# Performance work log

Measured on AMD Instinct MI355X. Metric: run time of the kernel, lower is better.

The kernel has to match this reference:

```python
import jax, jax.numpy as jnp
from jax import lax
import numpy as np

VOCAB = 36906
WORD_DIM = 300
HIDDEN = 200
B = 256
S = 256

def setup_inputs() -> dict:
    key = jax.random.key(0)
    ks = jax.random.split(key, 9)
    premise = jax.random.randint(ks[0], (B, S), 0, VOCAB)
    hypothesis = jax.random.randint(ks[1], (B, S), 0, VOCAB)
    s = 0.05
    emb = jax.random.normal(ks[2], (VOCAB, WORD_DIM), dtype=jnp.float32) * s
    W_ih = jax.random.normal(ks[3], (4 * HIDDEN, WORD_DIM), dtype=jnp.float32) * s
    W_hh = jax.random.normal(ks[4], (4 * HIDDEN, HIDDEN), dtype=jnp.float32) * s
    b_ih = jax.random.normal(ks[5], (4 * HIDDEN,), dtype=jnp.float32) * s
    b_hh = jax.random.normal(ks[6], (4 * HIDDEN,), dtype=jnp.float32) * s
    W_last = jax.random.normal(ks[7], (3, 4 * HIDDEN), dtype=jnp.float32) * s
    b_last = jax.random.normal(ks[8], (3,), dtype=jnp.float32) * s
    return {"premise": premise, "hypothesis": hypothesis, "emb": emb,
            "W_ih": W_ih, "W_hh": W_hh, "b_ih": b_ih, "b_hh": b_hh,
            "W_last": W_last, "b_last": b_last}

def _lstm_hidden_matrix(x_emb, W_ih, W_hh, b_ih, b_hh):
    # x_emb: [B, S, D] -> hidden states [B, S, H] (PyTorch LSTMCell math, zero init state)
    Bz = x_emb.shape[0]
    H = W_hh.shape[1]
    xs = jnp.swapaxes(x_emb, 0, 1)  # [S, B, D]
    h0 = jnp.zeros((Bz, H), x_emb.dtype)
    def step(carry, x_t):
        h, c = carry
        gates = x_t @ W_ih.T + b_ih + h @ W_hh.T + b_hh  # [B, 4H]
        i, f, g, o = jnp.split(gates, 4, axis=1)
        c = jax.nn.sigmoid(f) * c + jax.nn.sigmoid(i) * jnp.tanh(g)
        h = jax.nn.sigmoid(o) * jnp.tanh(c)
        return (h, c), h
    _, hs = lax.scan(step, (h0, h0), xs)
    return jnp.swapaxes(hs, 0, 1)  # [B, S, H]

def reference(premise, hypothesis, emb, W_ih, W_hh, b_ih, b_hh, W_last, b_last):
    _i = _lstm_hidden_matrix(emb[premise], W_ih, W_hh, b_ih, b_hh)      # [B, S, H]
    _t = _lstm_hidden_matrix(emb[hypothesis], W_ih, W_hh, b_ih, b_hh)  # [B, S, H]
    attn = jnp.einsum('bih,bjh->bij', _i, _t)          # [B, S, S]
    a1 = jax.nn.softmax(attn, axis=2)
    hq = jnp.max(jnp.einsum('bij,bjh->bih', a1, _t), axis=1)  # [B, H]
    a2 = jax.nn.softmax(jnp.swapaxes(attn, 1, 2), axis=2)
    hs = jnp.max(jnp.einsum('bji,bih->bjh', a2, _i), axis=1)  # [B, H]
    feat = jnp.concatenate([hq, hs, hq - hs, hq * hs], axis=1)  # [B, 4H]
    logits = feat @ W_last.T + b_last
    return jax.nn.log_softmax(logits, axis=1)
```

## Files before the change

kernel.cpp:

```cpp
#include <hip/hip_runtime.h>

typedef unsigned short u16;
typedef __attribute__((ext_vector_type(8))) __bf16 bf16x8;
typedef __attribute__((ext_vector_type(4))) float float4v;
typedef __attribute__((ext_vector_type(4))) u16 ushort4v;
typedef __attribute__((ext_vector_type(4))) unsigned int uint4v;

#define VOCAB 36906
#define VPAD  36928
#define WDP   320
#define HID   200
#define NG    800
#define NGP   832
#define KP    224
#define SS    256
#define ROWS  4
#define HS    232
#define GSF   804
#define WLS   228
#define NREG  5
#define NLDS  10

__device__ __forceinline__ float b2f(u16 u) {
  union { unsigned int i; float f; } c; c.i = ((unsigned int)u) << 16; return c.f;
}
__device__ __forceinline__ u16 f2b(float f) {
  union { float f; unsigned int i; } c; c.f = f;
  unsigned int u = c.i;
  u += 0x7fffu + ((u >> 16) & 1u);
  return (u16)(u >> 16);
}
__device__ __forceinline__ float sigm(float x) { return 1.f / (1.f + __expf(-x)); }
__device__ __forceinline__ float tanh_f(float x) {
  float e = __expf(2.f * x);
  return 1.f - 2.f / (e + 1.f);
}


__global__ void conv_emb(const float* __restrict__ emb, u16* __restrict__ out) {
  for (long long idx = (long long)blockIdx.x * 256 + threadIdx.x;
       idx < (long long)VPAD * WDP; idx += (long long)gridDim.x * 256) {
    int v = (int)(idx / WDP), k = (int)(idx % WDP);
    float val = (v < VOCAB && k < 300) ? emb[(long long)v * 300 + k] : 0.f;
    out[idx] = f2b(val);
  }
}

__global__ void conv_wih(const float* __restrict__ W, u16* __restrict__ out) {
  int idx = blockIdx.x * 256 + threadIdx.x;
  if (idx < NGP * WDP) {
    int n = idx / WDP, k = idx % WDP;
    float v = 0.f;
    if (n < NG && k < 300) { int gt = n & 3, j = n >> 2; v = W[(gt * HID + j) * 300 + k]; }
    out[idx] = f2b(v);
  }
}

__global__ void conv_whh(const float* __restrict__ W, u16* __restrict__ out) {
  int idx = blockIdx.x * 256 + threadIdx.x;
  if (idx < NG * KP) {
    int n = idx / KP, k = idx % KP;
    int gt = n & 3, j = n >> 2;
    float v = (k < HID) ? W[(gt * HID + j) * HID + k] : 0.f;
    out[idx] = f2b(v);
  }
}

__global__ void conv_bias(const float* __restrict__ bi, const float* __restrict__ bh,
                          float* __restrict__ out) {
  int n = blockIdx.x * 256 + threadIdx.x;
  if (n < NGP) {
    float v = 0.f;
    if (n < NG) { int gt = n & 3, j = n >> 2; v = bi[gt * HID + j] + bh[gt * HID + j]; }
    out[n] = v;
  }
}


__global__ __launch_bounds__(256, 2) void gemm_e2(
    const u16* __restrict__ A, const u16* __restrict__ B, u16* __restrict__ C,
    const float* __restrict__ bias) {
  __shared__ __align__(16) u16 La[64 * 40];
  __shared__ __align__(16) u16 Lb[64 * 40];
  const int m0 = blockIdx.x * 64, n0 = blockIdx.y * 64;
  const int tid = threadIdx.x, l = tid & 63, w = tid >> 6;
  const int wr = w >> 1, wc = w & 1;
  const int sr = tid >> 2, sc = (tid & 3) * 8;
  float4v acc[2][2] = {};
  for (int k0 = 0; k0 < WDP; k0 += 32) {
    uint4v qa = *(const uint4v*)&A[(long long)(m0 + sr) * WDP + k0 + sc];
    uint4v qb = *(const uint4v*)&B[(long long)(n0 + sr) * WDP + k0 + sc];
    __syncthreads();
    *(uint4v*)&La[sr * 40 + sc] = qa;
    *(uint4v*)&Lb[sr * 40 + sc] = qb;
    __syncthreads();
    bf16x8 af[2], bfr[2];
#pragma unroll
    for (int mt = 0; mt < 2; ++mt)
      af[mt] = *(const bf16x8*)&La[(wr * 32 + mt * 16 + (l & 15)) * 40 + (l >> 4) * 8];
#pragma unroll
    for (int nt = 0; nt < 2; ++nt)
      bfr[nt] = *(const bf16x8*)&Lb[(wc * 32 + nt * 16 + (l & 15)) * 40 + (l >> 4) * 8];
#pragma unroll
    for (int mt = 0; mt < 2; ++mt)
#pragma unroll
      for (int nt = 0; nt < 2; ++nt)
        acc[mt][nt] = __builtin_amdgcn_mfma_f32_16x16x32_bf16(af[mt], bfr[nt], acc[mt][nt], 0, 0, 0);
  }
#pragma unroll
  for (int mt = 0; mt < 2; ++mt)
#pragma unroll
    for (int nt = 0; nt < 2; ++nt)
#pragma unroll
      for (int j = 0; j < 4; ++j) {
        int row = m0 + wr * 32 + mt * 16 + (l >> 4) * 4 + j;
        int col = n0 + wc * 32 + nt * 16 + (l & 15);
        if (row < VOCAB && col < NG)
          C[(long long)row * NG + col] = f2b(acc[mt][nt][j] + bias[col]);
      }
}


__global__ __launch_bounds__(512, 2) void lstm_kernel(
    const int* __restrict__ premise, const int* __restrict__ hypothesis,
    const u16* __restrict__ E2, const u16* __restrict__ Whh,
    u16* __restrict__ hid) {
  __shared__ u16 tok[ROWS * 256];
  __shared__ __align__(16) u16 hbuf[16 * HS];
  __shared__ __align__(16) float gbufF[16 * GSF];
  __shared__ __align__(16) u16 wlds[NLDS * 16 * WLS];
  const int tid = threadIdx.x;
  const int l = tid & 63, w = tid >> 6;
  const int r0 = blockIdx.x * ROWS;

  for (int idx = tid; idx < ROWS * 256; idx += 512) {
    int mm = idx >> 8, tt = idx & 255;
    int row = r0 + mm;
    const int* seq = (row < 256) ? premise : hypothesis;
    tok[idx] = (u16)seq[(row & 255) * 256 + tt];
  }
  for (int idx = tid; idx < 16 * HS; idx += 512) hbuf[idx] = 0;
  for (int idx = tid; idx < NLDS * 16 * KP; idx += 512) {
    int slot = idx / (16 * KP), rem = idx % (16 * KP);
    int r = rem / KP, k = rem % KP;
    wlds[(slot * 16 + r) * WLS + k] = Whh[((40 + slot) * 16 + r) * KP + k];
  }

  uint4v wf[NREG][7];
#pragma unroll
  for (int i = 0; i < NREG; ++i) {
    int nt = w + 8 * i;
#pragma unroll
    for (int kf = 0; kf < 7; ++kf)
      wf[i][kf] = *(const uint4v*)&Whh[(nt * 16 + (l & 15)) * KP + kf * 32 + (l >> 4) * 8];
  }
#pragma unroll
  for (int i = 0; i < NREG; ++i)
#pragma unroll
    for (int kf = 0; kf < 7; ++kf)
      asm volatile("" : "+a"(wf[i][kf]));

  float cst[2];
  cst[0] = cst[1] = 0.f;

  ushort4v ev[2];
#pragma unroll
  for (int q = 0; q < 2; ++q) {
    int u = tid + 512 * q;
    if (u < ROWS * 200) {
      int m = u / 200, j = u - m * 200;
      int tk = tok[m * 256];
      ev[q] = *(const ushort4v*)&E2[(long long)tk * NG + 4 * j];
    }
  }
  __syncthreads();

  for (int t = 0; t < SS; ++t) {
    if (t > 0) {
      const unsigned* hb32 = (const unsigned*)hbuf;
      unsigned* hid32 = (unsigned*)hid;
      if (tid < ROWS * 112) {
        int m2 = tid / 112, c = tid - 112 * m2;
        hid32[((long long)(r0 + m2) * SS + (t - 1)) * 112 + c] = hb32[m2 * 116 + c];
      }
    }

    int t2 = (t < SS - 1) ? t + 1 : t;
    ushort4v evn[2];
#pragma unroll
    for (int q = 0; q < 2; ++q) {
      int u = tid + 512 * q;
      if (u < ROWS * 200) {
        int m = u / 200, j = u - m * 200;
        int tk = tok[m * 256 + t2];
        evn[q] = *(const ushort4v*)&E2[(long long)tk * NG + 4 * j];
      }
    }

    bf16x8 af[7];
#pragma unroll
    for (int kf = 0; kf < 7; ++kf)
      af[kf] = *(const bf16x8*)&hbuf[(l & 15) * HS + kf * 32 + (l >> 4) * 8];

    {
      float4v acc[NREG];
#pragma unroll
      for (int i = 0; i < NREG; ++i) acc[i] = float4v{0.f, 0.f, 0.f, 0.f};
      asm volatile("s_nop 1"
                   : "+v"(acc[0]), "+v"(acc[1]), "+v"(acc[2]), "+v"(acc[3]), "+v"(acc[4]));
#pragma unroll
      for (int kf = 0; kf < 7; ++kf)
#pragma unroll
        for (int i = 0; i < NREG; ++i)
          asm volatile("v_mfma_f32_16x16x32_bf16 %0, %1, %2, %0"
                       : "+v"(acc[i])
                       : "a"(wf[i][kf]), "v"(af[kf]));
      asm volatile("s_nop 7\n\ts_nop 7"
                   : "+v"(acc[0]), "+v"(acc[1]), "+v"(acc[2]), "+v"(acc[3]), "+v"(acc[4]));
#pragma unroll
      for (int i = 0; i < NREG; ++i) {
        int nt = w + 8 * i;
        *(float4v*)&gbufF[(l & 15) * GSF + nt * 16 + (l >> 4) * 4] = acc[i];
      }
    }
    {
      float4v a2 = {0.f, 0.f, 0.f, 0.f};
#pragma unroll
      for (int kf = 0; kf < 7; ++kf) {
        bf16x8 bfr = *(const bf16x8*)&wlds[(w * 16 + (l & 15)) * WLS + kf * 32 + (l >> 4) * 8];
        a2 = __builtin_amdgcn_mfma_f32_16x16x32_bf16(bfr, af[kf], a2, 0, 0, 0);
      }
      *(float4v*)&gbufF[(l & 15) * GSF + (40 + w) * 16 + (l >> 4) * 4] = a2;
    }
    if (w < 2) {
      int slot = 8 + w;
      float4v a2 = {0.f, 0.f, 0.f, 0.f};
#pragma unroll
      for (int kf = 0; kf < 7; ++kf) {
        bf16x8 bfr = *(const bf16x8*)&wlds[(slot * 16 + (l & 15)) * WLS + kf * 32 + (l >> 4) * 8];
        a2 = __builtin_amdgcn_mfma_f32_16x16x32_bf16(bfr, af[kf], a2, 0, 0, 0);
      }
      *(float4v*)&gbufF[(l & 15) * GSF + (48 + w) * 16 + (l >> 4) * 4] = a2;
    }
    __syncthreads();

#pragma unroll
    for (int q = 0; q < 2; ++q) {
      int u = tid + 512 * q;
      if (u < ROWS * 200) {
        int m = u / 200, j = u - m * 200;
        float4v gv = *(const float4v*)&gbufF[m * GSF + 4 * j];
        float gi = gv[0] + b2f(ev[q].x);
        float gf = gv[1] + b2f(ev[q].y);
        float gg = gv[2] + b2f(ev[q].z);
        float go = gv[3] + b2f(ev[q].w);
        float cn = sigm(gf) * cst[q] + sigm(gi) * tanh_f(gg);
        float hn = sigm(go) * tanh_f(cn);
        cst[q] = cn;
        hbuf[m * HS + j] = f2b(hn);
      }
    }
    ev[0] = evn[0]; ev[1] = evn[1];
    __syncthreads();
  }

  {
    const unsigned* hb32 = (const unsigned*)hbuf;
    unsigned* hid32 = (unsigned*)hid;
    if (tid < ROWS * 112) {
      int m2 = tid / 112, c = tid - 112 * m2;
      hid32[((long long)(r0 + m2) * SS + (SS - 1)) * 112 + c] = hb32[m2 * 116 + c];
    }
  }
}


__global__ __launch_bounds__(256, 2) void gemm_attn(const u16* __restrict__ H,
                                                    u16* __restrict__ X) {
  __shared__ __align__(16) u16 La[64 * 40];
  __shared__ __align__(16) u16 Lb[64 * 40];
  const int z = blockIdx.z;
  const u16* A = H + (long long)z * SS * KP;
  const u16* B = H + (long long)(z + 256) * SS * KP;
  u16* C = X + (long long)z * 65536;
  const int m0 = blockIdx.x * 64, n0 = blockIdx.y * 64;
  const int tid = threadIdx.x, l = tid & 63, w = tid >> 6;
  const int wr = w >> 1, wc = w & 1;
  const int sr = tid >> 2, sc = (tid & 3) * 8;
  float4v acc[2][2] = {};
  for (int k0 = 0; k0 < KP; k0 += 32) {
    uint4v qa = *(const uint4v*)&A[(m0 + sr) * KP + k0 + sc];
    uint4v qb = *(const uint4v*)&B[(n0 + sr) * KP + k0 + sc];
    __syncthreads();
    *(uint4v*)&La[sr * 40 + sc] = qa;
    *(uint4v*)&Lb[sr * 40 + sc] = qb;
    __syncthreads();
    bf16x8 af[2], bfr[2];
#pragma unroll
    for (int mt = 0; mt < 2; ++mt)
      af[mt] = *(const bf16x8*)&La[(wr * 32 + mt * 16 + (l & 15)) * 40 + (l >> 4) * 8];
#pragma unroll
    for (int nt = 0; nt < 2; ++nt)
      bfr[nt] = *(const bf16x8*)&Lb[(wc * 32 + nt * 16 + (l & 15)) * 40 + (l >> 4) * 8];
#pragma unroll
    for (int mt = 0; mt < 2; ++mt)
#pragma unroll
      for (int nt = 0; nt < 2; ++nt)
        acc[mt][nt] = __builtin_amdgcn_mfma_f32_16x16x32_bf16(af[mt], bfr[nt], acc[mt][nt], 0, 0, 0);
  }
#pragma unroll
  for (int mt = 0; mt < 2; ++mt)
#pragma unroll
    for (int nt = 0; nt < 2; ++nt)
#pragma unroll
      for (int j = 0; j < 4; ++j) {
        int row = m0 + wr * 32 + mt * 16 + (l >> 4) * 4 + j;
        int col = n0 + wc * 32 + nt * 16 + (l & 15);
        C[row * SS + col] = f2b(acc[mt][nt][j]);
      }
}


__global__ void rowstats(const u16* __restrict__ X, float* __restrict__ rm,
                         float* __restrict__ ri) {
  int r = blockIdx.x * 4 + (threadIdx.x >> 6);
  int l = threadIdx.x & 63;
  ushort4v q = *(const ushort4v*)(X + (long long)r * 256 + l * 4);
  float v0 = b2f(q.x), v1 = b2f(q.y), v2 = b2f(q.z), v3 = b2f(q.w);
  float m = fmaxf(fmaxf(v0, v1), fmaxf(v2, v3));
#pragma unroll
  for (int off = 32; off; off >>= 1) m = fmaxf(m, __shfl_xor(m, off));
  float s = __expf(v0 - m) + __expf(v1 - m) + __expf(v2 - m) + __expf(v3 - m);
#pragma unroll
  for (int off = 32; off; off >>= 1) s += __shfl_xor(s, off);
  if (l == 0) { rm[r] = m; ri[r] = 1.f / s; }
}

__global__ void colstats(const u16* __restrict__ X, float* __restrict__ cm,
                         float* __restrict__ ci) {
  int b = blockIdx.x, j0 = blockIdx.y * 16;
  int tid = threadIdx.x, jj = tid & 15, iq = tid >> 4;
  const u16* base = X + (long long)b * 65536;
  float v[16];
  float m = -1e30f;
#pragma unroll
  for (int ch = 0; ch < 16; ++ch) {
    v[ch] = b2f(base[(ch * 16 + iq) * 256 + j0 + jj]);
    m = fmaxf(m, v[ch]);
  }
  __shared__ float red[256];
  red[tid] = m; __syncthreads();
#pragma unroll
  for (int off = 128; off >= 16; off >>= 1) {
    if (tid < off) red[tid] = fmaxf(red[tid], red[tid + off]);
    __syncthreads();
  }
  float mm = red[jj]; __syncthreads();
  float s = 0.f;
#pragma unroll
  for (int ch = 0; ch < 16; ++ch) s += __expf(v[ch] - mm);
  red[tid] = s; __syncthreads();
#pragma unroll
  for (int off = 128; off >= 16; off >>= 1) {
    if (tid < off) red[tid] += red[tid + off];
    __syncthreads();
  }
  if (tid < 16) { cm[b * 256 + j0 + tid] = mm; ci[b * 256 + j0 + tid] = 1.f / red[tid]; }
}


template <int TRANSA>
__global__ __launch_bounds__(256, 2) void gemm_pv(
    const u16* __restrict__ X, const u16* __restrict__ H,
    const float* __restrict__ sm, const float* __restrict__ sinv,
    float* __restrict__ pmax) {
  __shared__ __align__(16) u16 La[64 * 40];
  __shared__ __align__(16) u16 Lb[64 * 40];
  __shared__ float red[8][64];
  const int z = blockIdx.z;
  const u16* Xz = X + (long long)z * 65536;
  const u16* B = H + (long long)(TRANSA ? z : z + 256) * SS * KP;
  const int m0 = blockIdx.x * 64, n0 = blockIdx.y * 64;
  const int tid = threadIdx.x, l = tid & 63, w = tid >> 6;
  const int wr = w >> 1, wc = w & 1;
  const int sr = tid >> 2, sc = (tid & 3) * 8;
  const int sr2 = tid >> 3, sc2 = (tid & 7) * 8;

  float m_s0 = 0.f, i_s0 = 0.f;
  float mj[8], ij[8];
  if (TRANSA == 0) {
    m_s0 = sm[z * 256 + m0 + sr];
    i_s0 = sinv[z * 256 + m0 + sr];
  } else {
#pragma unroll
    for (int e = 0; e < 8; ++e) {
      mj[e] = sm[z * 256 + m0 + sc2 + e];
      ij[e] = sinv[z * 256 + m0 + sc2 + e];
    }
  }

  float4v acc[2][2] = {};
  for (int k0 = 0; k0 < SS; k0 += 32) {
    union { uint4v v; u16 s[8]; } ua, ub;
    if (TRANSA == 0)
      ua.v = *(const uint4v*)&Xz[(m0 + sr) * SS + k0 + sc];
    else
      ua.v = *(const uint4v*)&Xz[(k0 + sr2) * SS + m0 + sc2];
    ub.v = *(const uint4v*)&B[(long long)(k0 + sr2) * KP + n0 + sc2];
    __syncthreads();
    if (TRANSA == 0) {
      u16 pa[8];
#pragma unroll
      for (int e = 0; e < 8; ++e)
        pa[e] = f2b(__expf(b2f(ua.s[e]) - m_s0) * i_s0);
      uint4v pk;
      pk.x = (unsigned)pa[0] | ((unsigned)pa[1] << 16);
      pk.y = (unsigned)pa[2] | ((unsigned)pa[3] << 16);
      pk.z = (unsigned)pa[4] | ((unsigned)pa[5] << 16);
      pk.w = (unsigned)pa[6] | ((unsigned)pa[7] << 16);
      *(uint4v*)&La[sr * 40 + sc] = pk;
    } else {
#pragma unroll
      for (int e = 0; e < 8; ++e)
        La[(sc2 + e) * 40 + sr2] = f2b(__expf(b2f(ua.s[e]) - mj[e]) * ij[e]);
    }
#pragma unroll
    for (int e = 0; e < 8; ++e)
      Lb[(sc2 + e) * 40 + sr2] = (n0 + sc2 + e < KP) ? ub.s[e] : (u16)0;
    __syncthreads();
    bf16x8 af[2], bfr[2];
#pragma unroll
    for (int mt = 0; mt < 2; ++mt)
      af[mt] = *(const bf16x8*)&La[(wr * 32 + mt * 16 + (l & 15)) * 40 + (l >> 4) * 8];
#pragma unroll
    for (int nt = 0; nt < 2; ++nt)
      bfr[nt] = *(const bf16x8*)&Lb[(wc * 32 + nt * 16 + (l & 15)) * 40 + (l >> 4) * 8];
#pragma unroll
    for (int mt = 0; mt < 2; ++mt)
#pragma unroll
      for (int nt = 0; nt < 2; ++nt)
        acc[mt][nt] = __builtin_amdgcn_mfma_f32_16x16x32_bf16(af[mt], bfr[nt], acc[mt][nt], 0, 0, 0);
  }
#pragma unroll
  for (int nt = 0; nt < 2; ++nt) {
    float v = -1e30f;
#pragma unroll
    for (int mt = 0; mt < 2; ++mt)
#pragma unroll
      for (int j = 0; j < 4; ++j) v = fmaxf(v, acc[mt][nt][j]);
    red[wr * 4 + (l >> 4)][wc * 32 + nt * 16 + (l & 15)] = v;
  }
  __syncthreads();
  if (tid < 64) {
    float m = red[0][tid];
#pragma unroll
    for (int g = 1; g < 8; ++g) m = fmaxf(m, red[g][tid]);
    pmax[((long long)z * 4 + blockIdx.x) * 256 + n0 + tid] = m;
  }
}

__global__ void maxfinal(const float* __restrict__ p1, const float* __restrict__ p2,
                         float* __restrict__ hq, float* __restrict__ hs) {
  int b = blockIdx.x, h = threadIdx.x;
  if (h < HID) {
    float m1 = -1e30f, m2 = -1e30f;
#pragma unroll
    for (int x = 0; x < 4; ++x) {
      m1 = fmaxf(m1, p1[(b * 4 + x) * 256 + h]);
      m2 = fmaxf(m2, p2[(b * 4 + x) * 256 + h]);
    }
    hq[b * HID + h] = m1;
    hs[b * HID + h] = m2;
  }
}


__global__ void final_k(const float* __restrict__ hq, const float* __restrict__ hs,
                        const float* __restrict__ Wl, const float* __restrict__ bl,
                        float* __restrict__ out) {
  int b = blockIdx.x, t = threadIdx.x;
  float a0 = 0.f, a1v = 0.f, a2v = 0.f;
  for (int hp = t; hp < 800; hp += 256) {
    int part = hp / 200, u = hp - part * 200;
    float q = hq[b * HID + u], s = hs[b * HID + u];
    float f = (part == 0) ? q : (part == 1) ? s : (part == 2) ? (q - s) : (q * s);
    a0 += f * Wl[hp]; a1v += f * Wl[800 + hp]; a2v += f * Wl[1600 + hp];
  }
#pragma unroll
  for (int off = 32; off; off >>= 1) {
    a0 += __shfl_xor(a0, off); a1v += __shfl_xor(a1v, off); a2v += __shfl_xor(a2v, off);
  }
  __shared__ float rr[12];
  int w = t >> 6;
  if ((t & 63) == 0) { rr[w] = a0; rr[4 + w] = a1v; rr[8 + w] = a2v; }
  __syncthreads();
  if (t == 0) {
    float l0 = rr[0] + rr[1] + rr[2] + rr[3] + bl[0];
    float l1 = rr[4] + rr[5] + rr[6] + rr[7] + bl[1];
    float l2 = rr[8] + rr[9] + rr[10] + rr[11] + bl[2];
    float mm = fmaxf(l0, fmaxf(l1, l2));
    float lse = mm + __logf(__expf(l0 - mm) + __expf(l1 - mm) + __expf(l2 - mm));
    out[b * 3 + 0] = l0 - lse;
    out[b * 3 + 1] = l1 - lse;
    out[b * 3 + 2] = l2 - lse;
  }
}


extern "C" void kernel_launch(void* const* d_in, const int* in_sizes, int n_in,
                              void* d_out, int out_size, void* d_ws, size_t ws_size,
                              hipStream_t stream) {
  const int* premise = (const int*)d_in[0];
  const int* hypothesis = (const int*)d_in[1];
  const float* emb = (const float*)d_in[2];
  const float* W_ih = (const float*)d_in[3];
  const float* W_hh = (const float*)d_in[4];
  const float* b_ih = (const float*)d_in[5];
  const float* b_hh = (const float*)d_in[6];
  const float* W_last = (const float*)d_in[7];
  const float* b_last = (const float*)d_in[8];
  float* out = (float*)d_out;

  char* ws = (char*)d_ws;
  const size_t O_hid  = 0;
  const size_t O_embB = 0;
  const size_t O_E2   = 58720256;
  const size_t O_X    = 58720256;
  const size_t O_rm   = 92274688;
  const size_t O_ri   = 92536832;
  const size_t O_cm   = 92798976;
  const size_t O_ci   = 93061120;
  const size_t O_p1   = 93323264;
  const size_t O_p2   = 94371840;
  const size_t O_hq   = 95420416;
  const size_t O_hs   = 95625216;
  const size_t O_whh  = 117769856;
  const size_t O_wih  = 118128256;
  const size_t O_bias = 118660736;

  u16* hid  = (u16*)(ws + O_hid);
  u16* embB = (u16*)(ws + O_embB);
  u16* E2   = (u16*)(ws + O_E2);
  u16* X    = (u16*)(ws + O_X);
  float* rm = (float*)(ws + O_rm);
  float* ri = (float*)(ws + O_ri);
  float* cm = (float*)(ws + O_cm);
  float* ci = (float*)(ws + O_ci);
  float* p1 = (float*)(ws + O_p1);
  float* p2 = (float*)(ws + O_p2);
  float* hq = (float*)(ws + O_hq);
  float* hs = (float*)(ws + O_hs);
  u16* whhB = (u16*)(ws + O_whh);
  u16* wihB = (u16*)(ws + O_wih);
  float* biasP = (float*)(ws + O_bias);

  conv_emb<<<4096, 256, 0, stream>>>(emb, embB);
  conv_wih<<<(NGP * WDP + 255) / 256, 256, 0, stream>>>(W_ih, wihB);
  conv_whh<<<(NG * KP + 255) / 256, 256, 0, stream>>>(W_hh, whhB);
  conv_bias<<<4, 256, 0, stream>>>(b_ih, b_hh, biasP);

  gemm_e2<<<dim3(VPAD / 64, NGP / 64), 256, 0, stream>>>(embB, wihB, E2, biasP);

  lstm_kernel<<<128, 512, 0, stream>>>(premise, hypothesis, E2, whhB, hid);

  gemm_attn<<<dim3(4, 4, 256), 256, 0, stream>>>(hid, X);

  rowstats<<<16384, 256, 0, stream>>>(X, rm, ri);
  colstats<<<dim3(256, 16), 256, 0, stream>>>(X, cm, ci);

  gemm_pv<0><<<dim3(4, 4, 256), 256, 0, stream>>>(X, hid, rm, ri, p1);
  gemm_pv<1><<<dim3(4, 4, 256), 256, 0, stream>>>(X, hid, cm, ci, p2);

  maxfinal<<<256, 256, 0, stream>>>(p1, p2, hq, hs);
  final_k<<<256, 256, 0, stream>>>(hq, hs, W_last, b_last, out);
}
```

Measured before the change: 752.4 us.

## Fuse LSTM gate math into MFMA epilogue with double-buffered hidden state

Drops the float gate staging buffer in LDS. Each wave now applies the LSTM cell update directly on its MFMA accumulator registers, for the rows that are real batch rows, and writes h into a ping-pong pair of hidden buffers. This removes one __syncthreads per timestep and the LDS round trip of the gate values. In exchange, only 4 of 16 lanes per wave do the activation math, and each thread carries seven cell states and seven embedding vectors, which adds register pressure.

```diff
diff --git a/kernel.cpp b/kernel.cpp
--- a/kernel.cpp
+++ b/kernel.cpp
@@ -16,7 +16,6 @@
 #define SS    256
 #define ROWS  4
 #define HS    232
-#define GSF   804
 #define WLS   228
 #define NREG  5
 #define NLDS  10
@@ -126,12 +125,13 @@
     const u16* __restrict__ E2, const u16* __restrict__ Whh,
     u16* __restrict__ hid) {
   __shared__ u16 tok[ROWS * 256];
-  __shared__ __align__(16) u16 hbuf[16 * HS];
-  __shared__ __align__(16) float gbufF[16 * GSF];
+  __shared__ __align__(16) u16 hb[2][16 * HS];
   __shared__ __align__(16) u16 wlds[NLDS * 16 * WLS];
   const int tid = threadIdx.x;
   const int l = tid & 63, w = tid >> 6;
   const int r0 = blockIdx.x * ROWS;
+  const int m = l & 15, grp = l >> 4;
+  const bool act = (m < ROWS);
 
   for (int idx = tid; idx < ROWS * 256; idx += 512) {
     int mm = idx >> 8, tt = idx & 255;
@@ -139,7 +139,7 @@
     const int* seq = (row < 256) ? premise : hypothesis;
     tok[idx] = (u16)seq[(row & 255) * 256 + tt];
   }
-  for (int idx = tid; idx < 16 * HS; idx += 512) hbuf[idx] = 0;
+  for (int idx = tid; idx < 2 * 16 * HS; idx += 512) ((u16*)hb)[idx] = 0;
   for (int idx = tid; idx < NLDS * 16 * KP; idx += 512) {
     int slot = idx / (16 * KP), rem = idx % (16 * KP);
     int r = rem / KP, k = rem % KP;
@@ -160,24 +160,29 @@
     for (int kf = 0; kf < 7; ++kf)
       asm volatile("" : "+a"(wf[i][kf]));
 
-  float cst[2];
-  cst[0] = cst[1] = 0.f;
-
-  ushort4v ev[2];
-#pragma unroll
-  for (int q = 0; q < 2; ++q) {
-    int u = tid + 512 * q;
-    if (u < ROWS * 200) {
-      int m = u / 200, j = u - m * 200;
-      int tk = tok[m * 256];
-      ev[q] = *(const ushort4v*)&E2[(long long)tk * NG + 4 * j];
-    }
-  }
+  float cst[7];
+#pragma unroll
+  for (int q = 0; q < 7; ++q) cst[q] = 0.f;
+
   __syncthreads();
 
+  ushort4v ev[7];
+  if (act) {
+    long long tk = tok[m * 256];
+#pragma unroll
+    for (int i = 0; i < NREG; ++i)
+      ev[i] = *(const ushort4v*)&E2[tk * NG + 4 * (4 * (w + 8 * i) + grp)];
+    ev[5] = *(const ushort4v*)&E2[tk * NG + 4 * (4 * (40 + w) + grp)];
+    if (w < 2)
+      ev[6] = *(const ushort4v*)&E2[tk * NG + 4 * (4 * (48 + w) + grp)];
+  }
+
   for (int t = 0; t < SS; ++t) {
+    const u16* hr = hb[(t & 1) ^ 1];
+    u16* hw = hb[t & 1];
+
     if (t > 0) {
-      const unsigned* hb32 = (const unsigned*)hbuf;
+      const unsigned* hb32 = (const unsigned*)hr;
       unsigned* hid32 = (unsigned*)hid;
       if (tid < ROWS * 112) {
         int m2 = tid / 112, c = tid - 112 * m2;
@@ -185,22 +190,22 @@
       }
     }
 
+    bf16x8 af[7];
+#pragma unroll
+    for (int kf = 0; kf < 7; ++kf)
+      af[kf] = *(const bf16x8*)&hr[(l & 15) * HS + kf * 32 + (l >> 4) * 8];
+
+    ushort4v evn[7];
     int t2 = (t < SS - 1) ? t + 1 : t;
-    ushort4v evn[2];
-#pragma unroll
-    for (int q = 0; q < 2; ++q) {
-      int u = tid + 512 * q;
-      if (u < ROWS * 200) {
-        int m = u / 200, j = u - m * 200;
-        int tk = tok[m * 256 + t2];
-        evn[q] = *(const ushort4v*)&E2[(long long)tk * NG + 4 * j];
-      }
-    }
-
-    bf16x8 af[7];
-#pragma unroll
-    for (int kf = 0; kf < 7; ++kf)
-      af[kf] = *(const bf16x8*)&hbuf[(l & 15) * HS + kf * 32 + (l >> 4) * 8];
+    if (act) {
+      long long tk = tok[m * 256 + t2];
+#pragma unroll
+      for (int i = 0; i < NREG; ++i)
+        evn[i] = *(const ushort4v*)&E2[tk * NG + 4 * (4 * (w + 8 * i) + grp)];
+      evn[5] = *(const ushort4v*)&E2[tk * NG + 4 * (4 * (40 + w) + grp)];
+      if (w < 2)
+        evn[6] = *(const ushort4v*)&E2[tk * NG + 4 * (4 * (48 + w) + grp)];
+    }
 
     {
       float4v acc[NREG];
@@ -217,10 +222,19 @@
                        : "a"(wf[i][kf]), "v"(af[kf]));
       asm volatile("s_nop 7\n\ts_nop 7"
                    : "+v"(acc[0]), "+v"(acc[1]), "+v"(acc[2]), "+v"(acc[3]), "+v"(acc[4]));
-#pragma unroll
-      for (int i = 0; i < NREG; ++i) {
-        int nt = w + 8 * i;
-        *(float4v*)&gbufF[(l & 15) * GSF + nt * 16 + (l >> 4) * 4] = acc[i];
+      if (act) {
+#pragma unroll
+        for (int i = 0; i < NREG; ++i) {
+          int u = 4 * (w + 8 * i) + grp;
+          float gi = acc[i][0] + b2f(ev[i].x);
+          float gf = acc[i][1] + b2f(ev[i].y);
+          float gg = acc[i][2] + b2f(ev[i].z);
+          float go = acc[i][3] + b2f(ev[i].w);
+          float cn = sigm(gf) * cst[i] + sigm(gi) * tanh_f(gg);
+          float hn = sigm(go) * tanh_f(cn);
+          cst[i] = cn;
+          hw[m * HS + u] = f2b(hn);
+        }
       }
     }
     {
@@ -230,7 +244,17 @@
         bf16x8 bfr = *(const bf16x8*)&wlds[(w * 16 + (l & 15)) * WLS + kf * 32 + (l >> 4) * 8];
         a2 = __builtin_amdgcn_mfma_f32_16x16x32_bf16(bfr, af[kf], a2, 0, 0, 0);
       }
-      *(float4v*)&gbufF[(l & 15) * GSF + (40 + w) * 16 + (l >> 4) * 4] = a2;
+      if (act) {
+        int u = 4 * (40 + w) + grp;
+        float gi = a2[0] + b2f(ev[5].x);
+        float gf = a2[1] + b2f(ev[5].y);
+        float gg = a2[2] + b2f(ev[5].z);
+        float go = a2[3] + b2f(ev[5].w);
+        float cn = sigm(gf) * cst[5] + sigm(gi) * tanh_f(gg);
+        float hn = sigm(go) * tanh_f(cn);
+        cst[5] = cn;
+        hw[m * HS + u] = f2b(hn);
+      }
     }
     if (w < 2) {
       int slot = 8 + w;
@@ -240,32 +264,26 @@
         bf16x8 bfr = *(const bf16x8*)&wlds[(slot * 16 + (l & 15)) * WLS + kf * 32 + (l >> 4) * 8];
         a2 = __builtin_amdgcn_mfma_f32_16x16x32_bf16(bfr, af[kf], a2, 0, 0, 0);
       }
-      *(float4v*)&gbufF[(l & 15) * GSF + (48 + w) * 16 + (l >> 4) * 4] = a2;
-    }
-    __syncthreads();
-
-#pragma unroll
-    for (int q = 0; q < 2; ++q) {
-      int u = tid + 512 * q;
-      if (u < ROWS * 200) {
-        int m = u / 200, j = u - m * 200;
-        float4v gv = *(const float4v*)&gbufF[m * GSF + 4 * j];
-        float gi = gv[0] + b2f(ev[q].x);
-        float gf = gv[1] + b2f(ev[q].y);
-        float gg = gv[2] + b2f(ev[q].z);
-        float go = gv[3] + b2f(ev[q].w);
-        float cn = sigm(gf) * cst[q] + sigm(gi) * tanh_f(gg);
+      if (act) {
+        int u = 4 * (48 + w) + grp;
+        float gi = a2[0] + b2f(ev[6].x);
+        float gf = a2[1] + b2f(ev[6].y);
+        float gg = a2[2] + b2f(ev[6].z);
+        float go = a2[3] + b2f(ev[6].w);
+        float cn = sigm(gf) * cst[6] + sigm(gi) * tanh_f(gg);
         float hn = sigm(go) * tanh_f(cn);
-        cst[q] = cn;
-        hbuf[m * HS + j] = f2b(hn);
-      }
-    }
-    ev[0] = evn[0]; ev[1] = evn[1];
+        cst[6] = cn;
+        hw[m * HS + u] = f2b(hn);
+      }
+    }
+
+#pragma unroll
+    for (int i = 0; i < 7; ++i) ev[i] = evn[i];
     __syncthreads();
   }
 
   {
-    const unsigned* hb32 = (const unsigned*)hbuf;
+    const unsigned* hb32 = (const unsigned*)hb[(SS - 1) & 1];
     unsigned* hid32 = (unsigned*)hid;
     if (tid < ROWS * 112) {
       int m2 = tid / 112, c = tid - 112 * m2;
```

Result: slower. 1.106 ms (+47.0%).
